# Optimization experiments

Measured on AMD Instinct MI355X. Metric: run time of the kernel, lower is better.

Reference implementation:

```python
import jax, jax.numpy as jnp
import numpy as np
from jax import lax

B, N, D = 4, 4096, 2048
E = 128            # expand_ratio = head dim
H = D // E         # 16 heads
CHUNK = 64
EPS = 1e-6


def setup_inputs() -> dict:
    key = jax.random.key(0)
    ks = jax.random.split(key, 6)
    std = 0.02
    x = jax.random.normal(ks[0], (B, N, D), dtype=jnp.float32)
    Wq = jax.random.normal(ks[1], (D, D), dtype=jnp.float32) * std
    Wk = jax.random.normal(ks[2], (D, D), dtype=jnp.float32) * std
    Wv = jax.random.normal(ks[3], (D, D), dtype=jnp.float32) * std
    Wo = jax.random.normal(ks[4], (D, D), dtype=jnp.float32) * std
    norm_w = jnp.ones((D,), dtype=jnp.float32)
    return {"x": x, "Wq": Wq, "Wk": Wk, "Wv": Wv, "Wo": Wo, "norm_w": norm_w}


def rmsnorm(x, w):
    var = jnp.mean(jnp.square(x), axis=-1, keepdims=True)
    return x * lax.rsqrt(var + EPS) * w


def chunked_gla(q, v, log_f):
    """Gated linear attention with per-channel ('vector') decay.

    Recurrence (per batch b, head h):
        S_t = diag(f_t) S_{t-1} + outer(k_t, v_t),  k_t = 1 - f_t = 1 - exp(log_f_t)
        o_t = q_t @ S_t
    Computed with an IO-aware chunked scan (intra-chunk matmul + inter-chunk state).
    q, v, log_f: [B, N, H, E] -> returns o: [B, N, H, E]
    """
    b, n, h, e = q.shape
    nc = n // CHUNK
    k = 1.0 - jnp.exp(log_f)

    def to_chunks(t):  # [B,N,H,E] -> [NC,B,C,H,E]
        return t.reshape(b, nc, CHUNK, h, e).transpose(1, 0, 2, 3, 4)

    qs, ks_, vs, lfs = map(to_chunks, (q, k, v, log_f))
    A = jnp.cumsum(lfs, axis=2)  # inclusive cumulative log-decay within chunk
    mask = jnp.tril(jnp.ones((CHUNK, CHUNK), dtype=bool))  # causal within chunk

    def step(S, xs):
        qc, kc, vc, Ac = xs            # [B,C,H,E]; S: [B,H,E,E]
        q_dec = qc * jnp.exp(Ac)       # q_t * prod_{r<=t} f_r
        k_dec = kc * jnp.exp(-Ac)
        # intra-chunk: scores[t,s] = <q_t * exp(A_t - A_s), k_s>, causal
        scores = jnp.einsum('bthe,bshe->bhts', q_dec, k_dec)
        scores = jnp.where(mask[None, None], scores, 0.0)
        o_intra = jnp.einsum('bhts,bshe->bthe', scores, vc)
        # inter-chunk: decayed query against carried state
        o_inter = jnp.einsum('bthe,bhef->bthf', q_dec, S)
        # state update to end of chunk
        A_last = Ac[:, -1]                              # [B,H,E]
        k_rem = kc * jnp.exp(A_last[:, None] - Ac)      # decay from s to chunk end
        S_new = jnp.exp(A_last)[..., None] * S + jnp.einsum('bthe,bthf->bhef', k_rem, vc)
        return S_new, o_intra + o_inter

    S0 = jnp.zeros((b, h, e, e), dtype=q.dtype)
    _, o = lax.scan(step, S0, (qs, ks_, vs, A))
    return o.transpose(1, 0, 2, 3, 4).reshape(b, n, h, e)


def reference(x, Wq, Wk, Wv, Wo, norm_w):
    b, n, d = x.shape
    q = jax.nn.silu(x @ Wq.T)                 # q_act = silu
    f = jax.nn.sigmoid(x @ Wk.T)              # f = sigmoid(k_proj(x))
    log_f = jax.nn.log_sigmoid(f)             # as in source (lower_bound is None)
    v = x @ Wv.T
    q, v, log_f = (t.reshape(b, n, H, E) for t in (q, v, log_f))
    o = chunked_gla(q, v, log_f)              # [B,N,H,E]
    o = o.reshape(b, n, d)
    o = rmsnorm(o, norm_w)
    return o @ Wo.T
```

## Files before the change

### kernel.cpp

```cpp
#include <hip/hip_runtime.h>
#include <cstdint>
#include <cstddef>

#define EPI_NONE 0
#define EPI_SILU 1
#define EPI_LOGSIG 2

typedef __attribute__((ext_vector_type(8))) short bf16x8;
typedef __attribute__((ext_vector_type(4))) float f32x4;

__device__ __forceinline__ float us2f(unsigned short u) {
    unsigned int x = ((unsigned int)u) << 16;
    return __uint_as_float(x);
}
__device__ __forceinline__ unsigned short f2us(float f) {
    unsigned int x = __float_as_uint(f);
    unsigned int r = (x + 0x7fffu + ((x >> 16) & 1u)) >> 16;
    return (unsigned short)r;
}

__device__ __forceinline__ void gl_lds16(const unsigned short* g, unsigned short* l) {
    __builtin_amdgcn_global_load_lds(
        (const __attribute__((address_space(1))) void*)g,
        (__attribute__((address_space(3))) void*)l, 16, 0, 0);
}

__global__ __launch_bounds__(256) void cast_bf16(const float* __restrict__ in,
                                                 unsigned short* __restrict__ out, int n8)
{
    int i = blockIdx.x * blockDim.x + threadIdx.x;
    if (i >= n8) return;
    const float4* p = (const float4*)(in + (size_t)i * 8);
    float4 a = p[0], b = p[1];
    __align__(16) unsigned short u[8];
    u[0] = f2us(a.x); u[1] = f2us(a.y); u[2] = f2us(a.z); u[3] = f2us(a.w);
    u[4] = f2us(b.x); u[5] = f2us(b.y); u[6] = f2us(b.z); u[7] = f2us(b.w);
    *(uint4*)(out + (size_t)i * 8) = *(const uint4*)u;
}

template<int EPI, bool OUT_BF16>
__global__ __launch_bounds__(256) void gemm_bt_mfma(const unsigned short* __restrict__ A,
                                                    const unsigned short* __restrict__ B,
                                                    void* __restrict__ Cv,
                                                    int M, int N, int K)
{
    __shared__ unsigned short smem[17408];
    unsigned short* As = smem;
    unsigned short* Bs = smem + 8192;

    const int tid  = threadIdx.x;
    const int lane = tid & 63;
    const int wv   = tid >> 6;
    const int m0   = blockIdx.x * 128;
    const int n0   = blockIdx.y * 128;
    const int wr   = (wv >> 1) * 64;
    const int wc   = (wv & 1) * 64;

    const int lrow8 = lane >> 3;
    const int xcol  = ((lane & 7) ^ lrow8) << 3;
    const unsigned short* Ag[4];
    const unsigned short* Bg[4];
    unsigned short* Al[4];
    unsigned short* Bl[4];
#pragma unroll
    for (int j = 0; j < 4; ++j) {
        const int seg = j * 4 + wv;
        const int row = seg * 8 + lrow8;
        Ag[j] = A + (size_t)(m0 + row) * K + xcol;
        Bg[j] = B + (size_t)(n0 + row) * K + xcol;
        Al[j] = As + seg * 512;
        Bl[j] = Bs + seg * 512;
    }

    f32x4 acc[4][4];
#pragma unroll
    for (int i = 0; i < 4; ++i)
#pragma unroll
        for (int j = 0; j < 4; ++j) acc[i][j] = (f32x4){0.f, 0.f, 0.f, 0.f};

    const int fr = lane & 15;
    const int fq = lane >> 4;
    const int rx = fr & 7;

    for (int k0 = 0; k0 < K; k0 += 64) {
        __syncthreads();
#pragma unroll
        for (int j = 0; j < 4; ++j) {
            gl_lds16(Ag[j] + k0, Al[j]);
            gl_lds16(Bg[j] + k0, Bl[j]);
        }
        __syncthreads();

#pragma unroll
        for (int ks = 0; ks < 2; ++ks) {
            const int ka = (((ks << 2) + fq) ^ rx) << 3;
            bf16x8 af[4], bfv[4];
#pragma unroll
            for (int ti = 0; ti < 4; ++ti)
                af[ti] = *(const bf16x8*)&As[(wr + ti * 16 + fr) * 64 + ka];
#pragma unroll
            for (int tj = 0; tj < 4; ++tj)
                bfv[tj] = *(const bf16x8*)&Bs[(wc + tj * 16 + fr) * 64 + ka];
#pragma unroll
            for (int ti = 0; ti < 4; ++ti)
#pragma unroll
                for (int tj = 0; tj < 4; ++tj)
                    acc[ti][tj] = __builtin_amdgcn_mfma_f32_16x16x32_bf16(
                        af[ti], bfv[tj], acc[ti][tj], 0, 0, 0);
        }
    }

    const int crow = (lane >> 4) * 4;
    const int ccol = lane & 15;

    if (OUT_BF16) {
        __syncthreads();
        unsigned short* Cs = smem;
#pragma unroll
        for (int ti = 0; ti < 4; ++ti)
#pragma unroll
            for (int r = 0; r < 4; ++r)
#pragma unroll
                for (int tj = 0; tj < 4; ++tj) {
                    float z = acc[ti][tj][r];
                    if (EPI == EPI_SILU) {
                        z = z / (1.f + __expf(-z));
                    } else if (EPI == EPI_LOGSIG) {
                        float s = 1.f / (1.f + __expf(-z));
                        z = -log1pf(__expf(-s));
                    }
                    Cs[(wr + ti * 16 + crow + r) * 136 + wc + tj * 16 + ccol] = f2us(z);
                }
        __syncthreads();
        const int row = tid >> 1, half = tid & 1;
        const unsigned short* src = &Cs[row * 136 + half * 64];
        unsigned short* dst = (unsigned short*)Cv + (size_t)(m0 + row) * N + n0 + half * 64;
#pragma unroll
        for (int i = 0; i < 8; ++i)
            *(uint4*)(dst + i * 8) = *(const uint4*)(src + i * 8);
    } else {
        float* C = (float*)Cv;
#pragma unroll
        for (int ti = 0; ti < 4; ++ti)
#pragma unroll
            for (int r = 0; r < 4; ++r) {
                const int row = m0 + wr + ti * 16 + crow + r;
#pragma unroll
                for (int tj = 0; tj < 4; ++tj) {
                    float z = acc[ti][tj][r];
                    if (EPI == EPI_SILU) {
                        z = z / (1.f + __expf(-z));
                    } else if (EPI == EPI_LOGSIG) {
                        float s = 1.f / (1.f + __expf(-z));
                        z = -log1pf(__expf(-s));
                    }
                    C[(size_t)row * N + n0 + wc + tj * 16 + ccol] = z;
                }
            }
    }
}

__global__ __launch_bounds__(256) void gla_a1(unsigned short* __restrict__ qb,
                                              unsigned short* __restrict__ lfb,
                                              const unsigned short* __restrict__ vb,
                                              unsigned short* __restrict__ obf,
                                              float* __restrict__ dbuf)
{
    __shared__ unsigned short q_sh[64][136];
    __shared__ unsigned short kd_sh[64][136];
    __shared__ unsigned short vT[128][72];
    __shared__ unsigned short sc[64][72];

    const int tid = threadIdx.x;
    const int bid = blockIdx.x;
    const int c = bid >> 6, bh = bid & 63;
    const int b = bh >> 4, h = bh & 15;
    const size_t tok0 = ((size_t)b * 4096 + (size_t)c * 64) * 2048 + (size_t)h * 128;

#pragma unroll
    for (int k = 0; k < 4; ++k) {
        int vi = tid + k * 256;
        int t = vi >> 4, e8 = (vi & 15) << 3;
        *(uint4*)&q_sh[t][e8]  = *(const uint4*)(qb  + tok0 + (size_t)t * 2048 + e8);
        *(uint4*)&kd_sh[t][e8] = *(const uint4*)(lfb + tok0 + (size_t)t * 2048 + e8);
    }
    if (tid < 128) {
        int t8 = tid >> 4, f8 = tid & 15;
        __align__(16) unsigned short a[8][8];
#pragma unroll
        for (int r = 0; r < 8; ++r)
            *(uint4*)a[r] = *(const uint4*)(vb + tok0 + (size_t)(t8 * 8 + r) * 2048 + f8 * 8);
#pragma unroll
        for (int j = 0; j < 8; ++j) {
            __align__(16) unsigned short w8[8];
#pragma unroll
            for (int r = 0; r < 8; ++r) w8[r] = a[r][j];
            *(uint4*)&vT[f8 * 8 + j][t8 * 8] = *(const uint4*)w8;
        }
    }
    __syncthreads();
    if (tid < 128) {
        const int e = tid;
        float a = 0.f;
        for (int t = 0; t < 64; ++t) {
            float lf = us2f(kd_sh[t][e]);
            a += lf;
            q_sh[t][e]  = f2us(us2f(q_sh[t][e]) * __expf(a));
            kd_sh[t][e] = f2us((1.f - __expf(lf)) * __expf(-a));
        }
        dbuf[(size_t)bid * 128 + e] = __expf(a);
    }
    __syncthreads();
#pragma unroll
    for (int k = 0; k < 4; ++k) {
        int vi = tid + k * 256;
        int t = vi >> 4, e8 = (vi & 15) << 3;
        *(uint4*)(qb  + tok0 + (size_t)t * 2048 + e8) = *(const uint4*)&q_sh[t][e8];
        *(uint4*)(lfb + tok0 + (size_t)t * 2048 + e8) = *(const uint4*)&kd_sh[t][e8];
    }

    const int lane = tid & 63, w = tid >> 6;
    const int fr = lane & 15, fq = lane >> 4;

    f32x4 sacc[4];
#pragma unroll
    for (int j = 0; j < 4; ++j) sacc[j] = (f32x4){0.f, 0.f, 0.f, 0.f};
#pragma unroll
    for (int ke = 0; ke < 4; ++ke) {
        bf16x8 af = *(const bf16x8*)&q_sh[16 * w + fr][ke * 32 + fq * 8];
#pragma unroll
        for (int tj = 0; tj < 4; ++tj) {
            bf16x8 bfv = *(const bf16x8*)&kd_sh[16 * tj + fr][ke * 32 + fq * 8];
            sacc[tj] = __builtin_amdgcn_mfma_f32_16x16x32_bf16(af, bfv, sacc[tj], 0, 0, 0);
        }
    }
#pragma unroll
    for (int tj = 0; tj < 4; ++tj)
#pragma unroll
        for (int r = 0; r < 4; ++r) {
            int trow = 16 * w + fq * 4 + r;
            int scol = 16 * tj + fr;
            sc[trow][scol] = f2us(scol <= trow ? sacc[tj][r] : 0.f);
        }
    __syncthreads();
    f32x4 oacc[8];
#pragma unroll
    for (int j = 0; j < 8; ++j) oacc[j] = (f32x4){0.f, 0.f, 0.f, 0.f};
#pragma unroll
    for (int ks = 0; ks < 2; ++ks) {
        bf16x8 af = *(const bf16x8*)&sc[16 * w + fr][ks * 32 + fq * 8];
#pragma unroll
        for (int tf = 0; tf < 8; ++tf) {
            bf16x8 bfv = *(const bf16x8*)&vT[16 * tf + fr][ks * 32 + fq * 8];
            oacc[tf] = __builtin_amdgcn_mfma_f32_16x16x32_bf16(af, bfv, oacc[tf], 0, 0, 0);
        }
    }
#pragma unroll
    for (int tf = 0; tf < 8; ++tf) {
        __align__(8) unsigned short o4[4];
#pragma unroll
        for (int r = 0; r < 4; ++r) o4[r] = f2us(oacc[tf][r]);
        *(uint2*)(obf + (((size_t)bid * 4 + w) * 8 + tf) * 256 + lane * 4) = *(const uint2*)o4;
    }
}

__global__ __launch_bounds__(256) void gla_a2(const unsigned short* __restrict__ lfb,
                                              const unsigned short* __restrict__ vb,
                                              const float* __restrict__ dbuf,
                                              unsigned short* __restrict__ UT)
{
    __shared__ unsigned short vT[128][72];
    __shared__ unsigned short kdT[128][72];
    __shared__ float d_sh[128];

    const int tid = threadIdx.x;
    const int bid = blockIdx.x;
    const int c = bid >> 6, bh = bid & 63;
    const int b = bh >> 4, h = bh & 15;
    const size_t tok0 = ((size_t)b * 4096 + (size_t)c * 64) * 2048 + (size_t)h * 128;

    if (tid < 128) {
        int t8 = tid >> 4, f8 = tid & 15;
        __align__(16) unsigned short a[8][8];
#pragma unroll
        for (int r = 0; r < 8; ++r)
            *(uint4*)a[r] = *(const uint4*)(vb + tok0 + (size_t)(t8 * 8 + r) * 2048 + f8 * 8);
#pragma unroll
        for (int j = 0; j < 8; ++j) {
            __align__(16) unsigned short w8[8];
#pragma unroll
            for (int r = 0; r < 8; ++r) w8[r] = a[r][j];
            *(uint4*)&vT[f8 * 8 + j][t8 * 8] = *(const uint4*)w8;
        }
        d_sh[tid] = dbuf[(size_t)bid * 128 + tid];
    } else {
        int i = tid - 128;
        int t8 = i >> 4, e8b = i & 15;
        __align__(16) unsigned short a[8][8];
#pragma unroll
        for (int r = 0; r < 8; ++r)
            *(uint4*)a[r] = *(const uint4*)(lfb + tok0 + (size_t)(t8 * 8 + r) * 2048 + e8b * 8);
#pragma unroll
        for (int j = 0; j < 8; ++j) {
            __align__(16) unsigned short w8[8];
#pragma unroll
            for (int r = 0; r < 8; ++r) w8[r] = a[r][j];
            *(uint4*)&kdT[e8b * 8 + j][t8 * 8] = *(const uint4*)w8;
        }
    }
    __syncthreads();

    const int lane = tid & 63, w = tid >> 6;
    const int fr = lane & 15, fq = lane >> 4;

    f32x4 acc[2][8];
#pragma unroll
    for (int mi = 0; mi < 2; ++mi)
#pragma unroll
        for (int te = 0; te < 8; ++te) acc[mi][te] = (f32x4){0.f, 0.f, 0.f, 0.f};
#pragma unroll
    for (int kt = 0; kt < 2; ++kt) {
        bf16x8 af0 = *(const bf16x8*)&vT[16 * (2 * w + 0) + fr][kt * 32 + fq * 8];
        bf16x8 af1 = *(const bf16x8*)&vT[16 * (2 * w + 1) + fr][kt * 32 + fq * 8];
#pragma unroll
        for (int te = 0; te < 8; ++te) {
            bf16x8 bfv = *(const bf16x8*)&kdT[16 * te + fr][kt * 32 + fq * 8];
            acc[0][te] = __builtin_amdgcn_mfma_f32_16x16x32_bf16(af0, bfv, acc[0][te], 0, 0, 0);
            acc[1][te] = __builtin_amdgcn_mfma_f32_16x16x32_bf16(af1, bfv, acc[1][te], 0, 0, 0);
        }
    }
    unsigned short* up = UT + (size_t)bid * 16384;
#pragma unroll
    for (int mi = 0; mi < 2; ++mi)
#pragma unroll
        for (int te = 0; te < 8; ++te) {
            int e = 16 * te + fr;
            float dv = d_sh[e];
#pragma unroll
            for (int r = 0; r < 4; ++r) {
                int f = 32 * w + 16 * mi + fq * 4 + r;
                up[f * 128 + e] = f2us(acc[mi][te][r] * dv);
            }
        }
}

__global__ __launch_bounds__(256) void gla_scan(unsigned short* __restrict__ UT,
                                                const float* __restrict__ dbuf)
{
    const int tid = threadIdx.x;
    const int bh = blockIdx.x >> 3, fs = blockIdx.x & 7;
    const int f = fs * 16 + (tid >> 4);
    const int e8 = (tid & 15) << 3;
    float S[8];
#pragma unroll
    for (int j = 0; j < 8; ++j) S[j] = 0.f;
    for (int c = 0; c < 64; ++c) {
        const size_t cb = (size_t)(c * 64 + bh);
        const size_t loc = cb * 16384 + (size_t)f * 128 + e8;
        uint4 uu = *(const uint4*)(UT + loc);
        float4 d0 = *(const float4*)(dbuf + cb * 128 + e8);
        float4 d1 = *(const float4*)(dbuf + cb * 128 + e8 + 4);
        __align__(16) unsigned short us8[8];
        *(uint4*)us8 = uu;
        __align__(16) unsigned short so[8];
#pragma unroll
        for (int j = 0; j < 8; ++j) so[j] = f2us(S[j]);
        *(uint4*)(UT + loc) = *(const uint4*)so;
        float dd[8] = {d0.x, d0.y, d0.z, d0.w, d1.x, d1.y, d1.z, d1.w};
#pragma unroll
        for (int j = 0; j < 8; ++j) S[j] = fmaf(dd[j], S[j], us2f(us8[j]));
    }
}

__global__ __launch_bounds__(256) void gla_c(unsigned short* __restrict__ qb,
                                             const unsigned short* __restrict__ UT,
                                             const unsigned short* __restrict__ obf)
{
    __shared__ unsigned short q_sh[64][136];
    __shared__ unsigned short ST_sh[128][136];

    const int tid = threadIdx.x;
    const int bid = blockIdx.x;
    const int c = bid >> 6, bh = bid & 63;
    const int b = bh >> 4, h = bh & 15;
    const size_t tok0 = ((size_t)b * 4096 + (size_t)c * 64) * 2048 + (size_t)h * 128;

#pragma unroll
    for (int k = 0; k < 4; ++k) {
        int vi = tid + k * 256;
        int t = vi >> 4, e8 = (vi & 15) << 3;
        *(uint4*)&q_sh[t][e8] = *(const uint4*)(qb + tok0 + (size_t)t * 2048 + e8);
    }
    const unsigned short* stp = UT + (size_t)bid * 16384;
#pragma unroll
    for (int k = 0; k < 8; ++k) {
        int vi = tid + k * 256;
        int f = vi >> 4, e8 = (vi & 15) << 3;
        *(uint4*)&ST_sh[f][e8] = *(const uint4*)(stp + (size_t)f * 128 + e8);
    }
    const int lane = tid & 63, w = tid >> 6;
    const int fr = lane & 15, fq = lane >> 4;

    f32x4 acc[8];
#pragma unroll
    for (int tf = 0; tf < 8; ++tf) {
        uint2 iv = *(const uint2*)(obf + (((size_t)bid * 4 + w) * 8 + tf) * 256 + lane * 4);
        __align__(8) unsigned short s4[4];
        *(uint2*)s4 = iv;
        acc[tf] = (f32x4){us2f(s4[0]), us2f(s4[1]), us2f(s4[2]), us2f(s4[3])};
    }
    __syncthreads();
#pragma unroll
    for (int ke = 0; ke < 4; ++ke) {
        bf16x8 af = *(const bf16x8*)&q_sh[16 * w + fr][ke * 32 + fq * 8];
#pragma unroll
        for (int tf = 0; tf < 8; ++tf) {
            bf16x8 bfv = *(const bf16x8*)&ST_sh[16 * tf + fr][ke * 32 + fq * 8];
            acc[tf] = __builtin_amdgcn_mfma_f32_16x16x32_bf16(af, bfv, acc[tf], 0, 0, 0);
        }
    }
#pragma unroll
    for (int tf = 0; tf < 8; ++tf)
#pragma unroll
        for (int r = 0; r < 4; ++r) {
            int t = 16 * w + fq * 4 + r;
            qb[tok0 + (size_t)t * 2048 + 16 * tf + fr] = f2us(acc[tf][r]);
        }
}

__global__ __launch_bounds__(256) void rmsnorm_kernel(unsigned short* __restrict__ o,
                                                      const float* __restrict__ w)
{
    __shared__ float red[4];
    const int row = blockIdx.x;
    const int tid = threadIdx.x;
    unsigned short* p = o + (size_t)row * 2048 + tid * 8;
    __align__(16) unsigned short u[8];
    *(uint4*)u = *(const uint4*)p;
    float f[8];
    float ss = 0.f;
#pragma unroll
    for (int j = 0; j < 8; ++j) { f[j] = us2f(u[j]); ss = fmaf(f[j], f[j], ss); }
#pragma unroll
    for (int off = 32; off > 0; off >>= 1) ss += __shfl_down(ss, off, 64);
    if ((tid & 63) == 0) red[tid >> 6] = ss;
    __syncthreads();
    float tot = red[0] + red[1] + red[2] + red[3];
    float scale = rsqrtf(tot * (1.f / 2048.f) + 1e-6f);
    const float* wp = w + tid * 8;
#pragma unroll
    for (int j = 0; j < 8; ++j) u[j] = f2us(f[j] * scale * wp[j]);
    *(uint4*)p = *(const uint4*)u;
}

extern "C" void kernel_launch(void* const* d_in, const int* in_sizes, int n_in,
                              void* d_out, int out_size, void* d_ws, size_t ws_size,
                              hipStream_t stream)
{
    const float* x  = (const float*)d_in[0];
    const float* Wq = (const float*)d_in[1];
    const float* Wk = (const float*)d_in[2];
    const float* Wv = (const float*)d_in[3];
    const float* Wo = (const float*)d_in[4];
    const float* nw = (const float*)d_in[5];
    float* out = (float*)d_out;

    const int M = 16384, N = 2048, K = 2048;
    const size_t S1 = (size_t)M * N;
    const size_t SW = (size_t)N * K;
    const size_t UTsz = (size_t)4096 * 16384;

    unsigned short* xb  = (unsigned short*)d_ws;
    unsigned short* Wqb = xb + S1;
    unsigned short* Wkb = Wqb + SW;
    unsigned short* Wvb = Wkb + SW;
    unsigned short* Wob = Wvb + SW;
    unsigned short* qb  = Wob + SW;
    unsigned short* vbf = qb + S1;
    unsigned short* lfb = vbf + S1;
    unsigned short* obf = lfb + S1;
    unsigned short* UT  = obf + S1;
    float* dbuf = (float*)(UT + UTsz);

    cast_bf16<<<(int)(S1 / 8 / 256), 256, 0, stream>>>(x, xb, (int)(S1 / 8));
    cast_bf16<<<(int)(SW / 8 / 256), 256, 0, stream>>>(Wq, Wqb, (int)(SW / 8));
    cast_bf16<<<(int)(SW / 8 / 256), 256, 0, stream>>>(Wk, Wkb, (int)(SW / 8));
    cast_bf16<<<(int)(SW / 8 / 256), 256, 0, stream>>>(Wv, Wvb, (int)(SW / 8));
    cast_bf16<<<(int)(SW / 8 / 256), 256, 0, stream>>>(Wo, Wob, (int)(SW / 8));

    dim3 gg(M / 128, N / 128);
    gemm_bt_mfma<EPI_SILU,  true><<<gg, 256, 0, stream>>>(xb, Wqb, qb,  M, N, K);
    gemm_bt_mfma<EPI_LOGSIG,true><<<gg, 256, 0, stream>>>(xb, Wkb, lfb, M, N, K);
    gemm_bt_mfma<EPI_NONE,  true><<<gg, 256, 0, stream>>>(xb, Wvb, vbf, M, N, K);

    gla_a1<<<4096, 256, 0, stream>>>(qb, lfb, vbf, obf, dbuf);
    gla_a2<<<4096, 256, 0, stream>>>(lfb, vbf, dbuf, UT);
    gla_scan<<<512, 256, 0, stream>>>(UT, dbuf);
    gla_c<<<4096, 256, 0, stream>>>(qb, UT, obf);

    rmsnorm_kernel<<<16384, 256, 0, stream>>>(qb, nw);
    gemm_bt_mfma<EPI_NONE, false><<<gg, 256, 0, stream>>>(qb, Wob, out, M, N, K);
}
```

Before: 1.357 ms.

## Rewrite GEMM as 256x256 double-buffered 8-wave pipeline with interleaved loads

Replaces the 128x128 single-buffered GEMM with a 256x256 tile, 512-thread kernel. Global-to-LDS loads for the next k-tiles are double-buffered and issued between four MFMA quadrant phases, with explicit vmcnt/lgkmcnt waits, barriers and setprio. The aim is to hide load latency behind matrix math and raise operand reuse. In exchange it uses 128KB of LDS and heavy register pressure, and the grid is smaller, which risks lower occupancy or tail imbalance.

```diff
diff --git a/kernel.cpp b/kernel.cpp
--- a/kernel.cpp
+++ b/kernel.cpp
@@ -23,6 +23,23 @@
     __builtin_amdgcn_global_load_lds(
         (const __attribute__((address_space(1))) void*)g,
         (__attribute__((address_space(3))) void*)l, 16, 0, 0);
+}
+
+#define BARR() asm volatile("s_barrier" ::: "memory")
+#define LGKM0() do { asm volatile("s_waitcnt lgkmcnt(0)" ::: "memory"); \
+                     __builtin_amdgcn_sched_barrier(0); } while (0)
+#define VMCNT(n) do { asm volatile("s_waitcnt vmcnt(" #n ")" ::: "memory"); \
+                      __builtin_amdgcn_sched_barrier(0); } while (0)
+
+template<int EPI>
+__device__ __forceinline__ float act(float z) {
+    if constexpr (EPI == EPI_SILU) {
+        return z / (1.f + __expf(-z));
+    } else if constexpr (EPI == EPI_LOGSIG) {
+        float s = 1.f / (1.f + __expf(-z));
+        return -log1pf(__expf(-s));
+    }
+    return z;
 }
 
 __global__ __launch_bounds__(256) void cast_bf16(const float* __restrict__ in,
@@ -38,124 +55,195 @@
     *(uint4*)(out + (size_t)i * 8) = *(const uint4*)u;
 }
 
+__device__ __forceinline__ void ld_a4(bf16x8 d[4][2], const unsigned short* buf,
+                                      int rowbase, int fr, int fq, int rx)
+{
+#pragma unroll
+    for (int t = 0; t < 4; ++t) {
+        const int row = rowbase + t * 16 + fr;
+#pragma unroll
+        for (int ks = 0; ks < 2; ++ks)
+            d[t][ks] = *(const bf16x8*)&buf[row * 64 + ((((ks << 2) + fq) ^ rx) << 3)];
+    }
+}
+__device__ __forceinline__ void ld_b2(bf16x8 d[2][2], const unsigned short* buf,
+                                      int rowbase, int fr, int fq, int rx)
+{
+#pragma unroll
+    for (int t = 0; t < 2; ++t) {
+        const int row = rowbase + t * 16 + fr;
+#pragma unroll
+        for (int ks = 0; ks < 2; ++ks)
+            d[t][ks] = *(const bf16x8*)&buf[row * 64 + ((((ks << 2) + fq) ^ rx) << 3)];
+    }
+}
+__device__ __forceinline__ void mma_q(f32x4 acc[8][4], const bf16x8 a[4][2], const bf16x8 b[2][2],
+                                      int ti0, int tj0)
+{
+#pragma unroll
+    for (int ks = 0; ks < 2; ++ks)
+#pragma unroll
+        for (int i = 0; i < 4; ++i)
+#pragma unroll
+            for (int j = 0; j < 2; ++j)
+                acc[ti0 + i][tj0 + j] = __builtin_amdgcn_mfma_f32_16x16x32_bf16(
+                    a[i][ks], b[j][ks], acc[ti0 + i][tj0 + j], 0, 0, 0);
+}
+
 template<int EPI, bool OUT_BF16>
-__global__ __launch_bounds__(256) void gemm_bt_mfma(const unsigned short* __restrict__ A,
-                                                    const unsigned short* __restrict__ B,
-                                                    void* __restrict__ Cv,
-                                                    int M, int N, int K)
-{
-    __shared__ unsigned short smem[17408];
-    unsigned short* As = smem;
-    unsigned short* Bs = smem + 8192;
+__global__ __launch_bounds__(512, 2) void gemm_bt_mfma(const unsigned short* __restrict__ A,
+                                                       const unsigned short* __restrict__ B,
+                                                       void* __restrict__ Cv,
+                                                       int M, int N, int K)
+{
+    __shared__ unsigned short smem[65536];
 
     const int tid  = threadIdx.x;
     const int lane = tid & 63;
     const int wv   = tid >> 6;
-    const int m0   = blockIdx.x * 128;
-    const int n0   = blockIdx.y * 128;
-    const int wr   = (wv >> 1) * 64;
-    const int wc   = (wv & 1) * 64;
-
-    const int lrow8 = lane >> 3;
-    const int xcol  = ((lane & 7) ^ lrow8) << 3;
-    const unsigned short* Ag[4];
-    const unsigned short* Bg[4];
-    unsigned short* Al[4];
-    unsigned short* Bl[4];
-#pragma unroll
-    for (int j = 0; j < 4; ++j) {
-        const int seg = j * 4 + wv;
-        const int row = seg * 8 + lrow8;
-        Ag[j] = A + (size_t)(m0 + row) * K + xcol;
-        Bg[j] = B + (size_t)(n0 + row) * K + xcol;
-        Al[j] = As + seg * 512;
-        Bl[j] = Bs + seg * 512;
-    }
-
-    f32x4 acc[4][4];
-#pragma unroll
-    for (int i = 0; i < 4; ++i)
+    const int m0   = blockIdx.x * 256;
+    const int n0   = blockIdx.y * 256;
+    const int wr   = (wv >> 2) * 128;
+    const int wc   = (wv & 3) * 64;
+    const int fr   = lane & 15;
+    const int fq   = lane >> 4;
+    const int rx   = fr & 7;
+    const int NT   = K >> 6;
+
+    unsigned short* const As0 = smem;
+    unsigned short* const Bs0 = smem + 16384;
+    unsigned short* const As1 = smem + 32768;
+    unsigned short* const Bs1 = smem + 49152;
+
+    const int srow = wv * 8 + (lane >> 3);
+    const int scol = ((lane & 7) ^ (lane >> 3)) << 3;
+    const unsigned short* Ag[2][2];
+    const unsigned short* Bg[2][2];
+#pragma unroll
+    for (int h = 0; h < 2; ++h)
+#pragma unroll
+        for (int i = 0; i < 2; ++i) {
+            Ag[h][i] = A + (size_t)(m0 + h * 128 + i * 64 + srow) * K + scol;
+            Bg[h][i] = B + (size_t)(n0 + h * 128 + i * 64 + srow) * K + scol;
+        }
+
+#define STAGE(gb, lb, h, Tt) do {                                         \
+        unsigned short* _l = (lb) + (h) * 8192 + wv * 512;                \
+        gl_lds16(gb[h][0] + (size_t)(Tt) * 64, _l);                       \
+        gl_lds16(gb[h][1] + (size_t)(Tt) * 64, _l + 4096);                \
+    } while (0)
+
+    f32x4 acc[8][4];
+#pragma unroll
+    for (int i = 0; i < 8; ++i)
 #pragma unroll
         for (int j = 0; j < 4; ++j) acc[i][j] = (f32x4){0.f, 0.f, 0.f, 0.f};
 
-    const int fr = lane & 15;
-    const int fq = lane >> 4;
-    const int rx = fr & 7;
-
-    for (int k0 = 0; k0 < K; k0 += 64) {
-        __syncthreads();
-#pragma unroll
-        for (int j = 0; j < 4; ++j) {
-            gl_lds16(Ag[j] + k0, Al[j]);
-            gl_lds16(Bg[j] + k0, Bl[j]);
-        }
-        __syncthreads();
-
-#pragma unroll
-        for (int ks = 0; ks < 2; ++ks) {
-            const int ka = (((ks << 2) + fq) ^ rx) << 3;
-            bf16x8 af[4], bfv[4];
-#pragma unroll
-            for (int ti = 0; ti < 4; ++ti)
-                af[ti] = *(const bf16x8*)&As[(wr + ti * 16 + fr) * 64 + ka];
-#pragma unroll
-            for (int tj = 0; tj < 4; ++tj)
-                bfv[tj] = *(const bf16x8*)&Bs[(wc + tj * 16 + fr) * 64 + ka];
-#pragma unroll
-            for (int ti = 0; ti < 4; ++ti)
-#pragma unroll
-                for (int tj = 0; tj < 4; ++tj)
-                    acc[ti][tj] = __builtin_amdgcn_mfma_f32_16x16x32_bf16(
-                        af[ti], bfv[tj], acc[ti][tj], 0, 0, 0);
-        }
-    }
-
-    const int crow = (lane >> 4) * 4;
-    const int ccol = lane & 15;
+    bf16x8 af[4][2], b0[2][2], b1[2][2];
+
+    STAGE(Ag, As0, 0, 0); STAGE(Ag, As0, 1, 0);
+    STAGE(Bg, Bs0, 0, 0); STAGE(Bg, Bs0, 1, 0);
+    STAGE(Bg, Bs1, 0, 1); STAGE(Bg, Bs1, 1, 1);
+    STAGE(Ag, As1, 0, 1);
+    VMCNT(6);
+    BARR();
+
+    for (int T = 0; T < NT; ++T) {
+        const int pb = T & 1;
+        unsigned short* const Ab  = smem + pb * 32768;
+        unsigned short* const Bb  = Ab + 16384;
+        unsigned short* const Anx = smem + (pb ^ 1) * 32768;
+
+        ld_a4(af, Ab, wr, fr, fq, rx);
+        ld_b2(b0, Bb, wc, fr, fq, rx);
+        if (T + 1 < NT) STAGE(Ag, Anx, 1, T + 1);
+        BARR(); LGKM0();
+        __builtin_amdgcn_s_setprio(1);
+        mma_q(acc, af, b0, 0, 0);
+        __builtin_amdgcn_s_setprio(0);
+        BARR();
+
+        ld_b2(b1, Bb, wc + 32, fr, fq, rx);
+        BARR(); LGKM0();
+        __builtin_amdgcn_s_setprio(1);
+        mma_q(acc, af, b1, 0, 2);
+        __builtin_amdgcn_s_setprio(0);
+        BARR();
+
+        ld_a4(af, Ab, wr + 64, fr, fq, rx);
+        if (T + 2 < NT) STAGE(Bg, Bb, 0, T + 2);
+        BARR(); LGKM0();
+        __builtin_amdgcn_s_setprio(1);
+        mma_q(acc, af, b0, 4, 0);
+        __builtin_amdgcn_s_setprio(0);
+        BARR();
+
+        if (T + 2 < NT) { STAGE(Bg, Bb, 1, T + 2); STAGE(Ag, Ab, 0, T + 2); }
+        if (T + 2 < NT)      { VMCNT(6); }
+        else if (T + 1 < NT) { VMCNT(0); }
+        BARR(); LGKM0();
+        __builtin_amdgcn_s_setprio(1);
+        mma_q(acc, af, b1, 4, 2);
+        __builtin_amdgcn_s_setprio(0);
+        BARR();
+    }
+#undef STAGE
+
+    const int crow = fq * 4;
+    const int ccol = fr;
 
     if (OUT_BF16) {
-        __syncthreads();
+        VMCNT(0);
         unsigned short* Cs = smem;
-#pragma unroll
-        for (int ti = 0; ti < 4; ++ti)
-#pragma unroll
-            for (int r = 0; r < 4; ++r)
-#pragma unroll
-                for (int tj = 0; tj < 4; ++tj) {
-                    float z = acc[ti][tj][r];
-                    if (EPI == EPI_SILU) {
-                        z = z / (1.f + __expf(-z));
-                    } else if (EPI == EPI_LOGSIG) {
-                        float s = 1.f / (1.f + __expf(-z));
-                        z = -log1pf(__expf(-s));
-                    }
-                    Cs[(wr + ti * 16 + crow + r) * 136 + wc + tj * 16 + ccol] = f2us(z);
-                }
-        __syncthreads();
-        const int row = tid >> 1, half = tid & 1;
-        const unsigned short* src = &Cs[row * 136 + half * 64];
-        unsigned short* dst = (unsigned short*)Cv + (size_t)(m0 + row) * N + n0 + half * 64;
-#pragma unroll
-        for (int i = 0; i < 8; ++i)
-            *(uint4*)(dst + i * 8) = *(const uint4*)(src + i * 8);
+        if (wr == 0) {
+#pragma unroll
+            for (int ti = 0; ti < 8; ++ti)
+#pragma unroll
+                for (int r = 0; r < 4; ++r)
+#pragma unroll
+                    for (int tj = 0; tj < 4; ++tj)
+                        Cs[(ti * 16 + crow + r) * 264 + wc + tj * 16 + ccol] =
+                            f2us(act<EPI>(acc[ti][tj][r]));
+        }
+        LGKM0(); BARR();
+        {
+            const int row = tid >> 2, cb = (tid & 3) << 6;
+            const unsigned short* src = &Cs[row * 264 + cb];
+            unsigned short* dst = (unsigned short*)Cv + (size_t)(m0 + row) * N + n0 + cb;
+#pragma unroll
+            for (int j = 0; j < 8; ++j)
+                *(uint4*)(dst + j * 8) = *(const uint4*)(src + j * 8);
+        }
+        BARR();
+        if (wr == 128) {
+#pragma unroll
+            for (int ti = 0; ti < 8; ++ti)
+#pragma unroll
+                for (int r = 0; r < 4; ++r)
+#pragma unroll
+                    for (int tj = 0; tj < 4; ++tj)
+                        Cs[(ti * 16 + crow + r) * 264 + wc + tj * 16 + ccol] =
+                            f2us(act<EPI>(acc[ti][tj][r]));
+        }
+        LGKM0(); BARR();
+        {
+            const int row = tid >> 2, cb = (tid & 3) << 6;
+            const unsigned short* src = &Cs[row * 264 + cb];
+            unsigned short* dst = (unsigned short*)Cv + (size_t)(m0 + 128 + row) * N + n0 + cb;
+#pragma unroll
+            for (int j = 0; j < 8; ++j)
+                *(uint4*)(dst + j * 8) = *(const uint4*)(src + j * 8);
+        }
     } else {
         float* C = (float*)Cv;
 #pragma unroll
-        for (int ti = 0; ti < 4; ++ti)
+        for (int ti = 0; ti < 8; ++ti)
 #pragma unroll
             for (int r = 0; r < 4; ++r) {
                 const int row = m0 + wr + ti * 16 + crow + r;
 #pragma unroll
-                for (int tj = 0; tj < 4; ++tj) {
-                    float z = acc[ti][tj][r];
-                    if (EPI == EPI_SILU) {
-                        z = z / (1.f + __expf(-z));
-                    } else if (EPI == EPI_LOGSIG) {
-                        float s = 1.f / (1.f + __expf(-z));
-                        z = -log1pf(__expf(-s));
-                    }
-                    C[(size_t)row * N + n0 + wc + tj * 16 + ccol] = z;
-                }
+                for (int tj = 0; tj < 4; ++tj)
+                    C[(size_t)row * N + n0 + wc + tj * 16 + ccol] = act<EPI>(acc[ti][tj][r]);
             }
     }
 }
@@ -488,10 +576,10 @@
     cast_bf16<<<(int)(SW / 8 / 256), 256, 0, stream>>>(Wv, Wvb, (int)(SW / 8));
     cast_bf16<<<(int)(SW / 8 / 256), 256, 0, stream>>>(Wo, Wob, (int)(SW / 8));
 
-    dim3 gg(M / 128, N / 128);
-    gemm_bt_mfma<EPI_SILU,  true><<<gg, 256, 0, stream>>>(xb, Wqb, qb,  M, N, K);
-    gemm_bt_mfma<EPI_LOGSIG,true><<<gg, 256, 0, stream>>>(xb, Wkb, lfb, M, N, K);
-    gemm_bt_mfma<EPI_NONE,  true><<<gg, 256, 0, stream>>>(xb, Wvb, vbf, M, N, K);
+    dim3 gg(M / 256, N / 256);
+    gemm_bt_mfma<EPI_SILU,  true><<<gg, 512, 0, stream>>>(xb, Wqb, qb,  M, N, K);
+    gemm_bt_mfma<EPI_LOGSIG,true><<<gg, 512, 0, stream>>>(xb, Wkb, lfb, M, N, K);
+    gemm_bt_mfma<EPI_NONE,  true><<<gg, 512, 0, stream>>>(xb, Wvb, vbf, M, N, K);
 
     gla_a1<<<4096, 256, 0, stream>>>(qb, lfb, vbf, obf, dbuf);
     gla_a2<<<4096, 256, 0, stream>>>(lfb, vbf, dbuf, UT);
@@ -499,5 +587,5 @@
     gla_c<<<4096, 256, 0, stream>>>(qb, UT, obf);
 
     rmsnorm_kernel<<<16384, 256, 0, stream>>>(qb, nw);
-    gemm_bt_mfma<EPI_NONE, false><<<gg, 256, 0, stream>>>(qb, Wob, out, M, N, K);
-}
+    gemm_bt_mfma<EPI_NONE, false><<<gg, 512, 0, stream>>>(qb, Wob, out, M, N, K);
+}
```

New measurement: 1.289 ms. -5.0%, faster.
